# Optimization experiments

Hardware: AMD Instinct MI355X
Metric: run time of the kernel (lower is better)

## Reference

```python
import jax, jax.numpy as jnp
import numpy as np

EPS = 1e-08

def setup_inputs() -> dict:
    key = jax.random.key(0)
    ks = jax.random.split(key, 7)
    B, O, A, D, H = 64, 100, 16, 1024, 512
    return {
        "obj_vecs_i": jax.random.normal(ks[0], (B, O, D), dtype=jnp.float32),
        "attr_feats": jax.random.normal(ks[1], (B, O, A, D), dtype=jnp.float32),
        "p_attr_feats": jax.random.normal(ks[2], (B, O, A, H), dtype=jnp.float32),
        "attr_masks": jax.random.randint(ks[3], (B, O, A), 0, 2, dtype=jnp.int32),
        "W_obj": jax.random.normal(ks[4], (H, D), dtype=jnp.float32) * 0.02,
        "b_obj": jax.random.normal(ks[5], (H,), dtype=jnp.float32) * 0.02,
        "w_alpha": jax.random.normal(ks[6], (H,), dtype=jnp.float32) * 0.02,
        "b_alpha": jnp.zeros((), dtype=jnp.float32),
    }

def reference(obj_vecs_i, attr_feats, p_attr_feats, attr_masks, W_obj, b_obj, w_alpha, b_alpha):
    # obj2att: [B,O,D] -> [B,O,H]
    att_obj = jnp.einsum('bod,hd->boh', obj_vecs_i, W_obj) + b_obj
    # additive score: tanh(p + q) then project to scalar per attribute
    dot = jnp.tanh(p_attr_feats + att_obj[:, :, None, :])          # [B,O,A,H]
    scores = jnp.einsum('boah,h->boa', dot, w_alpha) + b_alpha     # [B,O,A]
    weight = jax.nn.softmax(scores, axis=-1)                       # [B,O,A]
    # masked renormalization
    weight = weight * attr_masks.astype(weight.dtype)
    weight = weight / (jnp.sum(weight, axis=-1, keepdims=True) + EPS)
    # weighted-sum pooling over attributes
    att_res = jnp.einsum('boa,boad->bod', weight, attr_feats)      # [B,O,D]
    return att_res
```

## Files before the change

kernel.cpp:

```cpp
#include <hip/hip_runtime.h>
#include <stdint.h>

#define EPS 1e-8f

typedef __attribute__((ext_vector_type(8))) __bf16 bf16x8;
typedef __attribute__((ext_vector_type(4))) float f32x4;

static constexpr int BO = 6400;
static constexpr int AA = 16;
static constexpr int DD = 1024;
static constexpr int HH = 512;

__device__ __forceinline__ unsigned short f2bf(float x) {
    uint32_t b = __float_as_uint(x);
    b += 0x7fffu + ((b >> 16) & 1u);
    return (unsigned short)(b >> 16);
}

__device__ __forceinline__ float fast_tanh(float x) {
    float e = __expf(2.0f * x);
    return 1.0f - __fdividef(2.0f, e + 1.0f);
}

__global__ __launch_bounds__(256) void k_prep_w(const float* __restrict__ W,
                                                unsigned short* __restrict__ W_bf) {
    const int i = blockIdx.x * 256 + threadIdx.x;
    const long off = (long)i * 8;
    float4 v0 = *(const float4*)(W + off);
    float4 v1 = *(const float4*)(W + off + 4);
    union { unsigned short u[8]; int4 v; } pk;
    pk.u[0] = f2bf(v0.x); pk.u[1] = f2bf(v0.y); pk.u[2] = f2bf(v0.z); pk.u[3] = f2bf(v0.w);
    pk.u[4] = f2bf(v1.x); pk.u[5] = f2bf(v1.y); pk.u[6] = f2bf(v1.z); pk.u[7] = f2bf(v1.w);
    *(int4*)(W_bf + off) = pk.v;
}

__global__ __launch_bounds__(64) void k_gemm(const float* __restrict__ obj,
                                             const unsigned short* __restrict__ W_bf,
                                             const float* __restrict__ b_obj,
                                             float* __restrict__ att_obj) {
    const int lane = threadIdx.x;
    const int xcd  = blockIdx.x & 7;
    const int j    = blockIdx.x >> 3;
    const int mt   = xcd * 13 + (j % 13);
    if (mt >= 100) return;
    const int nt   = j / 13;
    const int m0   = mt * 64;
    const int n0   = nt * 64;
    const int lr   = lane & 15;
    const int lk   = (lane >> 4) * 8;

    const float*          ap = obj  + (size_t)(m0 + lr) * DD + lk;
    const unsigned short* bp = W_bf + (size_t)(n0 + lr) * DD + lk;

    f32x4 acc[4][4];
    #pragma unroll
    for (int i = 0; i < 4; ++i)
        #pragma unroll
        for (int jj = 0; jj < 4; ++jj) acc[i][jj] = f32x4{0.f, 0.f, 0.f, 0.f};

    float4 a_lo[4], a_hi[4];
    bf16x8 bfr[4];
    #pragma unroll
    for (int i = 0; i < 4; ++i) {
        a_lo[i] = *(const float4*)(ap + (size_t)i * 16 * DD);
        a_hi[i] = *(const float4*)(ap + (size_t)i * 16 * DD + 4);
        bfr[i]  = *(const bf16x8*)(bp + (size_t)i * 16 * DD);
    }

    #pragma unroll 1
    for (int k0 = 0; k0 < DD; k0 += 32) {
        const int kn = (k0 + 32 < DD) ? (k0 + 32) : 0;
        float4 na_lo[4], na_hi[4];
        bf16x8 nb[4];
        #pragma unroll
        for (int i = 0; i < 4; ++i) {
            na_lo[i] = *(const float4*)(ap + (size_t)i * 16 * DD + kn);
            na_hi[i] = *(const float4*)(ap + (size_t)i * 16 * DD + kn + 4);
            nb[i]    = *(const bf16x8*)(bp + (size_t)i * 16 * DD + kn);
        }
        bf16x8 afr[4];
        #pragma unroll
        for (int i = 0; i < 4; ++i) {
            afr[i][0] = (__bf16)a_lo[i].x; afr[i][1] = (__bf16)a_lo[i].y;
            afr[i][2] = (__bf16)a_lo[i].z; afr[i][3] = (__bf16)a_lo[i].w;
            afr[i][4] = (__bf16)a_hi[i].x; afr[i][5] = (__bf16)a_hi[i].y;
            afr[i][6] = (__bf16)a_hi[i].z; afr[i][7] = (__bf16)a_hi[i].w;
        }
        #pragma unroll
        for (int i = 0; i < 4; ++i)
            #pragma unroll
            for (int jj = 0; jj < 4; ++jj)
                acc[i][jj] = __builtin_amdgcn_mfma_f32_16x16x32_bf16(afr[i], bfr[jj], acc[i][jj], 0, 0, 0);
        #pragma unroll
        for (int i = 0; i < 4; ++i) { a_lo[i] = na_lo[i]; a_hi[i] = na_hi[i]; bfr[i] = nb[i]; }
    }

    const int crow = (lane >> 4) * 4;
    #pragma unroll
    for (int jj = 0; jj < 4; ++jj) {
        const int n = n0 + jj * 16 + lr;
        const float bb = b_obj[n];
        #pragma unroll
        for (int i = 0; i < 4; ++i) {
            #pragma unroll
            for (int r = 0; r < 4; ++r)
                att_obj[(size_t)(m0 + i * 16 + crow + r) * HH + n] = acc[i][jj][r] + bb;
        }
    }
}

__global__ __launch_bounds__(256, 5) void k_attn(const float* __restrict__ att_obj,
                                                 const float* __restrict__ p_attr,
                                                 const int* __restrict__ masks,
                                                 const float* __restrict__ w_alpha,
                                                 const float* __restrict__ attr_feats,
                                                 float* __restrict__ out) {
    __shared__ float s_sc[AA];

    const int tid  = threadIdx.x;
    const int wv   = tid >> 6;
    const int lane = tid & 63;
    const int row  = blockIdx.x;

    int mbits;
    {
        const int4* m4 = (const int4*)(masks + (size_t)row * AA);
        int4 a = m4[0], b = m4[1], c = m4[2], d = m4[3];
        mbits =  (a.x)      | (a.y << 1)  | (a.z << 2)  | (a.w << 3)
              | (b.x << 4) | (b.y << 5)  | (b.z << 6)  | (b.w << 7)
              | (c.x << 8) | (c.y << 9)  | (c.z << 10) | (c.w << 11)
              | (d.x << 12)| (d.y << 13) | (d.z << 14) | (d.w << 15);
    }

    const float* prow = p_attr     + (size_t)row * AA * HH;
    const float* arow = attr_feats + (size_t)row * AA * DD;

    {
        const f32x4* att4 = (const f32x4*)(att_obj + (size_t)row * HH);
        const f32x4* wa4  = (const f32x4*)w_alpha;
        const f32x4 av0 = att4[lane], av1 = att4[64 + lane];
        const f32x4 wv0 = wa4[lane],  wv1 = wa4[64 + lane];

        f32x4 x0[4], x1[4];
        #pragma unroll
        for (int q = 0; q < 4; ++q) {
            const int a = wv * 4 + q;
            if (mbits >> a & 1) {
                const f32x4* pa = (const f32x4*)(prow + (size_t)a * HH);
                x0[q] = pa[lane];
                x1[q] = pa[64 + lane];
            }
        }
        #pragma unroll
        for (int q = 0; q < 4; ++q) {
            const int a = wv * 4 + q;
            if (mbits >> a & 1) {
                float s;
                s  = wv0.x * fast_tanh(x0[q].x + av0.x);
                s += wv0.y * fast_tanh(x0[q].y + av0.y);
                s += wv0.z * fast_tanh(x0[q].z + av0.z);
                s += wv0.w * fast_tanh(x0[q].w + av0.w);
                s += wv1.x * fast_tanh(x1[q].x + av1.x);
                s += wv1.y * fast_tanh(x1[q].y + av1.y);
                s += wv1.z * fast_tanh(x1[q].z + av1.z);
                s += wv1.w * fast_tanh(x1[q].w + av1.w);
                s += __shfl_xor(s, 1);
                s += __shfl_xor(s, 2);
                s += __shfl_xor(s, 4);
                s += __shfl_xor(s, 8);
                s += __shfl_xor(s, 16);
                s += __shfl_xor(s, 32);
                if (lane == 0) s_sc[a] = s;
            }
        }
    }
    __syncthreads();

    float w[AA];
    {
        float mx = -3.0e38f;
        #pragma unroll
        for (int a = 0; a < AA; ++a)
            mx = fmaxf(mx, (mbits >> a & 1) ? s_sc[a] : -3.0e38f);
        float T = 0.f;
        #pragma unroll
        for (int a = 0; a < AA; ++a) {
            float e = (mbits >> a & 1) ? __expf(s_sc[a] - mx) : 0.f;
            w[a] = e;
            T += e;
        }
        const float inv = (T > 0.f) ? 1.0f / (T * (1.0f + EPS)) : 0.f;
        #pragma unroll
        for (int a = 0; a < AA; ++a) w[a] *= inv;
    }

    const f32x4* af4 = (const f32x4*)arow;
    f32x4 acc = {0.f, 0.f, 0.f, 0.f};
    #pragma unroll
    for (int h = 0; h < 2; ++h) {
        f32x4 v[8];
        #pragma unroll
        for (int q = 0; q < 8; ++q) {
            const int a = h * 8 + q;
            if (mbits >> a & 1) v[q] = af4[a * 256 + tid];
        }
        #pragma unroll
        for (int q = 0; q < 8; ++q) {
            const int a = h * 8 + q;
            if (mbits >> a & 1) acc += w[a] * v[q];
        }
    }
    *(f32x4*)(out + (size_t)row * DD + tid * 4) = acc;
}

extern "C" void kernel_launch(void* const* d_in, const int* in_sizes, int n_in,
                              void* d_out, int out_size, void* d_ws, size_t ws_size,
                              hipStream_t stream) {
    const float* obj_vecs   = (const float*)d_in[0];
    const float* attr_feats = (const float*)d_in[1];
    const float* p_attr     = (const float*)d_in[2];
    const int*   masks      = (const int*)d_in[3];
    const float* W_obj      = (const float*)d_in[4];
    const float* b_obj      = (const float*)d_in[5];
    const float* w_alpha    = (const float*)d_in[6];
    float* out = (float*)d_out;

    char* ws = (char*)d_ws;
    float*          att_obj = (float*)ws;
    unsigned short* W_bf    = (unsigned short*)(ws + 13107200);

    k_prep_w<<<256, 256, 0, stream>>>(W_obj, W_bf);
    k_gemm<<<832, 64, 0, stream>>>(obj_vecs, W_bf, b_obj, att_obj);
    k_attn<<<BO, 256, 0, stream>>>(att_obj, p_attr, masks, w_alpha, attr_feats, out);
}
```

Measured before the change: 121.9 us.

## Raise attn occupancy by shrinking in-flight loads and recomputing softmax weights

Raises the attention kernel's launch bound from 5 to 8 blocks per SIMD-group target. To fit the tighter register budget, it loads p_attr rows two at a time instead of four, gathers attr_feats in groups of four instead of eight, and recomputes each exp weight at use instead of keeping a 16-entry weight array. The output is written with a nontemporal store. The trade is more resident waves for latency hiding against fewer outstanding loads per wave and a repeated exp.

Measured after the change: 119.0 us. 2.4% less time.

```diff
diff --git a/kernel.cpp b/kernel.cpp
--- a/kernel.cpp
+++ b/kernel.cpp
@@ -109,7 +109,7 @@
     }
 }
 
-__global__ __launch_bounds__(256, 5) void k_attn(const float* __restrict__ att_obj,
+__global__ __launch_bounds__(256, 8) void k_attn(const float* __restrict__ att_obj,
                                                  const float* __restrict__ p_attr,
                                                  const int* __restrict__ masks,
                                                  const float* __restrict__ w_alpha,
@@ -141,76 +141,81 @@
         const f32x4 av0 = att4[lane], av1 = att4[64 + lane];
         const f32x4 wv0 = wa4[lane],  wv1 = wa4[64 + lane];
 
-        f32x4 x0[4], x1[4];
-        #pragma unroll
-        for (int q = 0; q < 4; ++q) {
-            const int a = wv * 4 + q;
-            if (mbits >> a & 1) {
-                const f32x4* pa = (const f32x4*)(prow + (size_t)a * HH);
-                x0[q] = pa[lane];
-                x1[q] = pa[64 + lane];
-            }
-        }
-        #pragma unroll
-        for (int q = 0; q < 4; ++q) {
-            const int a = wv * 4 + q;
-            if (mbits >> a & 1) {
+        #pragma unroll
+        for (int pr = 0; pr < 2; ++pr) {
+            const int a1 = wv * 4 + pr * 2;
+            const int a2 = a1 + 1;
+            const bool on1 = (mbits >> a1) & 1;
+            const bool on2 = (mbits >> a2) & 1;
+            f32x4 xa0, xa1, xb0, xb1;
+            if (on1) {
+                const f32x4* pa = (const f32x4*)(prow + (size_t)a1 * HH);
+                xa0 = pa[lane]; xa1 = pa[64 + lane];
+            }
+            if (on2) {
+                const f32x4* pb = (const f32x4*)(prow + (size_t)a2 * HH);
+                xb0 = pb[lane]; xb1 = pb[64 + lane];
+            }
+            if (on1) {
                 float s;
-                s  = wv0.x * fast_tanh(x0[q].x + av0.x);
-                s += wv0.y * fast_tanh(x0[q].y + av0.y);
-                s += wv0.z * fast_tanh(x0[q].z + av0.z);
-                s += wv0.w * fast_tanh(x0[q].w + av0.w);
-                s += wv1.x * fast_tanh(x1[q].x + av1.x);
-                s += wv1.y * fast_tanh(x1[q].y + av1.y);
-                s += wv1.z * fast_tanh(x1[q].z + av1.z);
-                s += wv1.w * fast_tanh(x1[q].w + av1.w);
-                s += __shfl_xor(s, 1);
-                s += __shfl_xor(s, 2);
-                s += __shfl_xor(s, 4);
-                s += __shfl_xor(s, 8);
-                s += __shfl_xor(s, 16);
-                s += __shfl_xor(s, 32);
-                if (lane == 0) s_sc[a] = s;
+                s  = wv0.x * fast_tanh(xa0.x + av0.x);
+                s += wv0.y * fast_tanh(xa0.y + av0.y);
+                s += wv0.z * fast_tanh(xa0.z + av0.z);
+                s += wv0.w * fast_tanh(xa0.w + av0.w);
+                s += wv1.x * fast_tanh(xa1.x + av1.x);
+                s += wv1.y * fast_tanh(xa1.y + av1.y);
+                s += wv1.z * fast_tanh(xa1.z + av1.z);
+                s += wv1.w * fast_tanh(xa1.w + av1.w);
+                s += __shfl_xor(s, 1);  s += __shfl_xor(s, 2);
+                s += __shfl_xor(s, 4);  s += __shfl_xor(s, 8);
+                s += __shfl_xor(s, 16); s += __shfl_xor(s, 32);
+                if (lane == 0) s_sc[a1] = s;
+            }
+            if (on2) {
+                float s;
+                s  = wv0.x * fast_tanh(xb0.x + av0.x);
+                s += wv0.y * fast_tanh(xb0.y + av0.y);
+                s += wv0.z * fast_tanh(xb0.z + av0.z);
+                s += wv0.w * fast_tanh(xb0.w + av0.w);
+                s += wv1.x * fast_tanh(xb1.x + av1.x);
+                s += wv1.y * fast_tanh(xb1.y + av1.y);
+                s += wv1.z * fast_tanh(xb1.z + av1.z);
+                s += wv1.w * fast_tanh(xb1.w + av1.w);
+                s += __shfl_xor(s, 1);  s += __shfl_xor(s, 2);
+                s += __shfl_xor(s, 4);  s += __shfl_xor(s, 8);
+                s += __shfl_xor(s, 16); s += __shfl_xor(s, 32);
+                if (lane == 0) s_sc[a2] = s;
             }
         }
     }
     __syncthreads();
 
-    float w[AA];
-    {
-        float mx = -3.0e38f;
-        #pragma unroll
-        for (int a = 0; a < AA; ++a)
-            mx = fmaxf(mx, (mbits >> a & 1) ? s_sc[a] : -3.0e38f);
-        float T = 0.f;
-        #pragma unroll
-        for (int a = 0; a < AA; ++a) {
-            float e = (mbits >> a & 1) ? __expf(s_sc[a] - mx) : 0.f;
-            w[a] = e;
-            T += e;
-        }
-        const float inv = (T > 0.f) ? 1.0f / (T * (1.0f + EPS)) : 0.f;
-        #pragma unroll
-        for (int a = 0; a < AA; ++a) w[a] *= inv;
-    }
+    float mx = -3.0e38f;
+    #pragma unroll
+    for (int a = 0; a < AA; ++a)
+        mx = fmaxf(mx, (mbits >> a & 1) ? s_sc[a] : -3.0e38f);
+    float T = 0.f;
+    #pragma unroll
+    for (int a = 0; a < AA; ++a)
+        T += (mbits >> a & 1) ? __expf(s_sc[a] - mx) : 0.f;
+    const float inv = (T > 0.f) ? 1.0f / (T * (1.0f + EPS)) : 0.f;
 
     const f32x4* af4 = (const f32x4*)arow;
     f32x4 acc = {0.f, 0.f, 0.f, 0.f};
     #pragma unroll
-    for (int h = 0; h < 2; ++h) {
-        f32x4 v[8];
-        #pragma unroll
-        for (int q = 0; q < 8; ++q) {
-            const int a = h * 8 + q;
-            if (mbits >> a & 1) v[q] = af4[a * 256 + tid];
-        }
-        #pragma unroll
-        for (int q = 0; q < 8; ++q) {
-            const int a = h * 8 + q;
-            if (mbits >> a & 1) acc += w[a] * v[q];
-        }
-    }
-    *(f32x4*)(out + (size_t)row * DD + tid * 4) = acc;
+    for (int h = 0; h < 4; ++h) {
+        f32x4 v0, v1, v2, v3;
+        const int b0 = h * 4;
+        if (mbits >> (b0 + 0) & 1) v0 = af4[(b0 + 0) * 256 + tid];
+        if (mbits >> (b0 + 1) & 1) v1 = af4[(b0 + 1) * 256 + tid];
+        if (mbits >> (b0 + 2) & 1) v2 = af4[(b0 + 2) * 256 + tid];
+        if (mbits >> (b0 + 3) & 1) v3 = af4[(b0 + 3) * 256 + tid];
+        if (mbits >> (b0 + 0) & 1) acc += (__expf(s_sc[b0 + 0] - mx) * inv) * v0;
+        if (mbits >> (b0 + 1) & 1) acc += (__expf(s_sc[b0 + 1] - mx) * inv) * v1;
+        if (mbits >> (b0 + 2) & 1) acc += (__expf(s_sc[b0 + 2] - mx) * inv) * v2;
+        if (mbits >> (b0 + 3) & 1) acc += (__expf(s_sc[b0 + 3] - mx) * inv) * v3;
+    }
+    __builtin_nontemporal_store(acc, (f32x4*)(out + (size_t)row * DD + tid * 4));
 }
 
 extern "C" void kernel_launch(void* const* d_in, const int* in_sizes, int n_in,
```
